# Optimization experiments

Measured on AMD Instinct MI355X. Metric: run time of the kernel, lower is better.

## Reference

```python
import jax, jax.numpy as jnp
import numpy as np

NUM_EMB = 32      # max_num_embodiments
ACTION_DIM = 32
HID = 1536        # hidden_size == input_embedding_dim
B, T = 32, 32


def sinusoidal_pos_encoding(pos, dim):
    # pos: (..., ) float positions; returns (..., dim) with interleaved sin/cos
    half = dim // 2
    div = jnp.exp(-jnp.log(10000.0) * jnp.arange(half, dtype=jnp.float32) / half)
    args = pos[..., None].astype(jnp.float32) * div  # (..., half)
    pe = jnp.stack([jnp.sin(args), jnp.cos(args)], axis=-1)  # (..., half, 2)
    return pe.reshape(*pos.shape, dim)


def cat_linear(x, W, b, cat_ids):
    # x: (B,T,Din); W: (C,Din,Dout); b: (C,Dout); cat_ids: (B,)
    # faithful to torch: gather per-sample weights then batched matmul
    Wc = W[cat_ids]                      # (B,Din,Dout)
    bc = b[cat_ids]                      # (B,Dout)
    return jnp.einsum('btd,bdh->bth', x, Wc) + bc[:, None, :]


def setup_inputs() -> dict:
    key = jax.random.key(0)
    ks = jax.random.split(key, 10)
    actions = jax.random.normal(ks[0], (B, T, ACTION_DIM), dtype=jnp.float32)
    timesteps = jax.random.randint(ks[1], (B,), 0, 1000, dtype=jnp.int32)
    cat_ids = jax.random.randint(ks[2], (B,), 0, NUM_EMB, dtype=jnp.int32)
    W1 = 0.02 * jax.random.normal(ks[3], (NUM_EMB, ACTION_DIM, HID), dtype=jnp.float32)
    b1 = jnp.zeros((NUM_EMB, HID), dtype=jnp.float32)
    W2 = 0.02 * jax.random.normal(ks[4], (NUM_EMB, 2 * HID, HID), dtype=jnp.float32)
    b2 = jnp.zeros((NUM_EMB, HID), dtype=jnp.float32)
    W3 = 0.02 * jax.random.normal(ks[5], (NUM_EMB, HID, HID), dtype=jnp.float32)
    b3 = jnp.zeros((NUM_EMB, HID), dtype=jnp.float32)
    return {"actions": actions, "timesteps": timesteps, "cat_ids": cat_ids,
            "W1": W1, "b1": b1, "W2": W2, "b2": b2, "W3": W3, "b3": b3}


def reference(actions, timesteps, cat_ids, W1, b1, W2, b2, W3, b3):
    # timesteps (B,) -> (B,T)
    ts = jnp.broadcast_to(timesteps[:, None], (actions.shape[0], actions.shape[1]))
    a_emb = cat_linear(actions, W1, b1, cat_ids)               # (B,T,HID)
    tau_emb = sinusoidal_pos_encoding(ts, HID).astype(a_emb.dtype)  # (B,T,HID)
    x = jnp.concatenate([a_emb, tau_emb], axis=-1)             # (B,T,2*HID)
    h = cat_linear(x, W2, b2, cat_ids)
    h = h * jax.nn.sigmoid(h)  # swish
    return cat_linear(h, W3, b3, cat_ids)                      # (B,T,HID)
```

## Files before the change

kernel.cpp:

```cpp
#include <hip/hip_runtime.h>
#include <hip/hip_bf16.h>
#include <cstdint>
#include <cstddef>

#define HIDD 1536
#define NB 32
#define NT 32
#define AD 32

typedef __attribute__((ext_vector_type(8))) __bf16 bf16x8;
typedef __attribute__((ext_vector_type(4))) float floatx4;

__device__ __forceinline__ unsigned short f2bf(float f) {
    union { float f; uint32_t u; } v; v.f = f;
    uint32_t r = v.u + 0x7fffu + ((v.u >> 16) & 1u);
    return (unsigned short)(r >> 16);
}

__device__ __forceinline__ uint32_t pack2(float lo, float hi) {
    return (uint32_t)f2bf(lo) | ((uint32_t)f2bf(hi) << 16);
}

__global__ __launch_bounds__(256) void build_x_kernel(
    const float* __restrict__ actions,
    const int*   __restrict__ timesteps,
    const int*   __restrict__ cat_ids,
    const float* __restrict__ W1,
    const float* __restrict__ b1,
    unsigned short* __restrict__ Xout)
{
    const int b = blockIdx.z, t = blockIdx.y;
    const int j = blockIdx.x * 256 + threadIdx.x;
    __shared__ float as[AD];
    if (threadIdx.x < AD) as[threadIdx.x] = actions[(b * NT + t) * AD + threadIdx.x];
    __syncthreads();

    float val;
    if (j < HIDD) {
        const int c = cat_ids[b];
        const float* w = W1 + ((size_t)c * AD) * HIDD + j;
        float acc = b1[c * HIDD + j];
        #pragma unroll
        for (int k = 0; k < AD; ++k) acc += as[k] * w[(size_t)k * HIDD];
        val = acc;
    } else {
        const int jj = j - HIDD;
        const int i = jj >> 1;
        const float div = expf(-9.210340371976184f * (float)i * (1.0f / 768.0f));
        const float arg = (float)timesteps[b] * div;
        val = (jj & 1) ? cosf(arg) : sinf(arg);
    }
    Xout[((size_t)(b * NT + t)) * (2 * HIDD) + j] = f2bf(val);
}

template<int K, bool SWISH>
__global__ __launch_bounds__(256) void gemm_cat_kernel(
    const unsigned short* __restrict__ X,
    const float* __restrict__ W,
    const float* __restrict__ bias,
    const int*   __restrict__ cat_ids,
    unsigned short* __restrict__ OutBf,
    float* __restrict__ OutF)
{
    const int b  = blockIdx.y;
    const int c  = cat_ids[b];
    const int n0 = blockIdx.x * 64;
    const int tid  = threadIdx.x;
    const int wave = tid >> 6;
    const int lane = tid & 63;

    __shared__ __align__(16) unsigned short Xs[32][72];
    __shared__ __align__(16) unsigned short Ws[64][72];

    floatx4 acc0 = {0.f, 0.f, 0.f, 0.f};
    floatx4 acc1 = {0.f, 0.f, 0.f, 0.f};

    const int xt = tid >> 3;
    const int xk = (tid & 7) * 8;

    const int wk_base = (tid >> 4) * 2;
    const int wn4     = (tid & 15) * 4;

    for (int kb = 0; kb < K / 64; ++kb) {
        {
            const uint4 xv = *reinterpret_cast<const uint4*>(
                X + ((size_t)(b * 32 + xt)) * K + kb * 64 + xk);
            *reinterpret_cast<uint4*>(&Xs[xt][xk]) = xv;
        }
        #pragma unroll
        for (int p = 0; p < 2; ++p) {
            const int k0 = wk_base + p * 32;
            const float* wsrc = W + ((size_t)c * K + (size_t)(kb * 64 + k0)) * HIDD + n0 + wn4;
            const float4 r0 = *reinterpret_cast<const float4*>(wsrc);
            const float4 r1 = *reinterpret_cast<const float4*>(wsrc + HIDD);
            *reinterpret_cast<uint32_t*>(&Ws[wn4 + 0][k0]) = pack2(r0.x, r1.x);
            *reinterpret_cast<uint32_t*>(&Ws[wn4 + 1][k0]) = pack2(r0.y, r1.y);
            *reinterpret_cast<uint32_t*>(&Ws[wn4 + 2][k0]) = pack2(r0.z, r1.z);
            *reinterpret_cast<uint32_t*>(&Ws[wn4 + 3][k0]) = pack2(r0.w, r1.w);
        }
        __syncthreads();

        #pragma unroll
        for (int ks = 0; ks < 2; ++ks) {
            const bf16x8 a0 = *reinterpret_cast<const bf16x8*>(
                &Xs[lane & 15][ks * 32 + (lane >> 4) * 8]);
            const bf16x8 a1 = *reinterpret_cast<const bf16x8*>(
                &Xs[16 + (lane & 15)][ks * 32 + (lane >> 4) * 8]);
            const bf16x8 bw = *reinterpret_cast<const bf16x8*>(
                &Ws[wave * 16 + (lane & 15)][ks * 32 + (lane >> 4) * 8]);
            acc0 = __builtin_amdgcn_mfma_f32_16x16x32_bf16(a0, bw, acc0, 0, 0, 0);
            acc1 = __builtin_amdgcn_mfma_f32_16x16x32_bf16(a1, bw, acc1, 0, 0, 0);
        }
        __syncthreads();
    }

    const int n_col = n0 + wave * 16 + (lane & 15);
    const float bv = bias[c * HIDD + n_col];
    const int quad = lane >> 4;
    #pragma unroll
    for (int r = 0; r < 4; ++r) {
        const int m0 = quad * 4 + r;
        float v0 = acc0[r] + bv;
        float v1 = acc1[r] + bv;
        if (SWISH) {
            v0 = v0 / (1.f + __expf(-v0));
            v1 = v1 / (1.f + __expf(-v1));
            OutBf[((size_t)(b * 32 + m0)) * HIDD + n_col] = f2bf(v0);
            OutBf[((size_t)(b * 32 + m0 + 16)) * HIDD + n_col] = f2bf(v1);
        } else {
            OutF[((size_t)(b * 32 + m0)) * HIDD + n_col] = v0;
            OutF[((size_t)(b * 32 + m0 + 16)) * HIDD + n_col] = v1;
        }
    }
}

extern "C" void kernel_launch(void* const* d_in, const int* in_sizes, int n_in,
                              void* d_out, int out_size, void* d_ws, size_t ws_size,
                              hipStream_t stream) {
    (void)in_sizes; (void)n_in; (void)out_size; (void)ws_size;
    const float* actions   = (const float*)d_in[0];
    const int*   timesteps = (const int*)d_in[1];
    const int*   cat_ids   = (const int*)d_in[2];
    const float* W1        = (const float*)d_in[3];
    const float* b1        = (const float*)d_in[4];
    const float* W2        = (const float*)d_in[5];
    const float* b2        = (const float*)d_in[6];
    const float* W3        = (const float*)d_in[7];
    const float* b3        = (const float*)d_in[8];
    float* out = (float*)d_out;

    unsigned short* xbuf = (unsigned short*)d_ws;
    unsigned short* hbuf = xbuf + (size_t)NB * NT * 2 * HIDD;

    build_x_kernel<<<dim3(12, NT, NB), 256, 0, stream>>>(
        actions, timesteps, cat_ids, W1, b1, xbuf);

    gemm_cat_kernel<2 * HIDD, true><<<dim3(24, NB), 256, 0, stream>>>(
        xbuf, W2, b2, cat_ids, hbuf, nullptr);

    gemm_cat_kernel<HIDD, false><<<dim3(24, NB), 256, 0, stream>>>(
        hbuf, W3, b3, cat_ids, nullptr, out);
}
```

Baseline: 918.4 us.

## Group samples by category so each weight tile is loaded once per group

After: 1.118 ms. 21.8% more time.

```diff
diff --git a/kernel.cpp b/kernel.cpp
--- a/kernel.cpp
+++ b/kernel.cpp
@@ -7,6 +7,8 @@
 #define NB 32
 #define NT 32
 #define AD 32
+#define NCAT 32
+#define MCHUNK 4
 
 typedef __attribute__((ext_vector_type(8))) __bf16 bf16x8;
 typedef __attribute__((ext_vector_type(4))) float floatx4;
@@ -19,6 +21,25 @@
 
 __device__ __forceinline__ uint32_t pack2(float lo, float hi) {
     return (uint32_t)f2bf(lo) | ((uint32_t)f2bf(hi) << 16);
+}
+
+__global__ void prep_kernel(const int* __restrict__ cat_ids, int* __restrict__ items) {
+    if (threadIdx.x == 0 && blockIdx.x == 0) {
+        int n = 0;
+        for (int c = 0; c < NCAT; ++c) {
+            int lst[NB]; int cnt = 0;
+            for (int b = 0; b < NB; ++b) if (cat_ids[b] == c) lst[cnt++] = b;
+            for (int off = 0; off < cnt; off += MCHUNK) {
+                int m = cnt - off; if (m > MCHUNK) m = MCHUNK;
+                items[n]      = c;
+                items[32 + n] = m;
+                for (int j = 0; j < MCHUNK; ++j)
+                    items[64 + n * 4 + j] = (j < m) ? lst[off + j] : 0;
+                ++n;
+            }
+        }
+        items[192] = n;
+    }
 }
 
 __global__ __launch_bounds__(256) void build_x_kernel(
@@ -54,82 +75,108 @@
 }
 
 template<int K, bool SWISH>
-__global__ __launch_bounds__(256) void gemm_cat_kernel(
+__global__ __launch_bounds__(256) void gemm_grouped_kernel(
     const unsigned short* __restrict__ X,
     const float* __restrict__ W,
     const float* __restrict__ bias,
-    const int*   __restrict__ cat_ids,
+    const int*   __restrict__ items,
     unsigned short* __restrict__ OutBf,
     float* __restrict__ OutF)
 {
-    const int b  = blockIdx.y;
-    const int c  = cat_ids[b];
-    const int n0 = blockIdx.x * 64;
+    const int it = blockIdx.y;
+    if (it >= items[192]) return;
+    const int c = items[it];
+    const int m = items[32 + it];
+    int smp[MCHUNK];
+    #pragma unroll
+    for (int j = 0; j < MCHUNK; ++j) smp[j] = items[64 + it * 4 + j];
+
+    const int n0   = blockIdx.x * 64;
     const int tid  = threadIdx.x;
     const int wave = tid >> 6;
     const int lane = tid & 63;
-
-    __shared__ __align__(16) unsigned short Xs[32][72];
+    const int quad = lane >> 4;
+    const int l16  = lane & 15;
+
     __shared__ __align__(16) unsigned short Ws[64][72];
 
-    floatx4 acc0 = {0.f, 0.f, 0.f, 0.f};
-    floatx4 acc1 = {0.f, 0.f, 0.f, 0.f};
-
-    const int xt = tid >> 3;
-    const int xk = (tid & 7) * 8;
-
-    const int wk_base = (tid >> 4) * 2;
-    const int wn4     = (tid & 15) * 4;
-
-    for (int kb = 0; kb < K / 64; ++kb) {
+    floatx4 acc[MCHUNK][2];
+    #pragma unroll
+    for (int si = 0; si < MCHUNK; ++si)
+        #pragma unroll
+        for (int rt = 0; rt < 2; ++rt)
+            acc[si][rt] = floatx4{0.f, 0.f, 0.f, 0.f};
+
+    const int q4 = (tid >> 4) * 4;
+    const int i4 = (tid & 15) * 4;
+    const float* wbase = W + (size_t)c * K * HIDD + n0 + i4;
+
+    constexpr int KT = K / 64;
+
+    float4 r0 = *reinterpret_cast<const float4*>(wbase + (size_t)(q4 + 0) * HIDD);
+    float4 r1 = *reinterpret_cast<const float4*>(wbase + (size_t)(q4 + 1) * HIDD);
+    float4 r2 = *reinterpret_cast<const float4*>(wbase + (size_t)(q4 + 2) * HIDD);
+    float4 r3 = *reinterpret_cast<const float4*>(wbase + (size_t)(q4 + 3) * HIDD);
+
+    for (int kb = 0; kb < KT; ++kb) {
+        __syncthreads();
         {
-            const uint4 xv = *reinterpret_cast<const uint4*>(
-                X + ((size_t)(b * 32 + xt)) * K + kb * 64 + xk);
-            *reinterpret_cast<uint4*>(&Xs[xt][xk]) = xv;
-        }
+            uint2 s0 = {pack2(r0.x, r1.x), pack2(r2.x, r3.x)};
+            uint2 s1 = {pack2(r0.y, r1.y), pack2(r2.y, r3.y)};
+            uint2 s2 = {pack2(r0.z, r1.z), pack2(r2.z, r3.z)};
+            uint2 s3 = {pack2(r0.w, r1.w), pack2(r2.w, r3.w)};
+            *reinterpret_cast<uint2*>(&Ws[i4 + 0][q4]) = s0;
+            *reinterpret_cast<uint2*>(&Ws[i4 + 1][q4]) = s1;
+            *reinterpret_cast<uint2*>(&Ws[i4 + 2][q4]) = s2;
+            *reinterpret_cast<uint2*>(&Ws[i4 + 3][q4]) = s3;
+        }
+        if (kb + 1 < KT) {
+            const float* wn = wbase + (size_t)((kb + 1) * 64 + q4) * HIDD;
+            r0 = *reinterpret_cast<const float4*>(wn);
+            r1 = *reinterpret_cast<const float4*>(wn + HIDD);
+            r2 = *reinterpret_cast<const float4*>(wn + 2 * HIDD);
+            r3 = *reinterpret_cast<const float4*>(wn + 3 * HIDD);
+        }
+        __syncthreads();
+
+        const bf16x8 bw0 = *reinterpret_cast<const bf16x8*>(&Ws[wave * 16 + l16][0 + quad * 8]);
+        const bf16x8 bw1 = *reinterpret_cast<const bf16x8*>(&Ws[wave * 16 + l16][32 + quad * 8]);
+
         #pragma unroll
-        for (int p = 0; p < 2; ++p) {
-            const int k0 = wk_base + p * 32;
-            const float* wsrc = W + ((size_t)c * K + (size_t)(kb * 64 + k0)) * HIDD + n0 + wn4;
-            const float4 r0 = *reinterpret_cast<const float4*>(wsrc);
-            const float4 r1 = *reinterpret_cast<const float4*>(wsrc + HIDD);
-            *reinterpret_cast<uint32_t*>(&Ws[wn4 + 0][k0]) = pack2(r0.x, r1.x);
-            *reinterpret_cast<uint32_t*>(&Ws[wn4 + 1][k0]) = pack2(r0.y, r1.y);
-            *reinterpret_cast<uint32_t*>(&Ws[wn4 + 2][k0]) = pack2(r0.z, r1.z);
-            *reinterpret_cast<uint32_t*>(&Ws[wn4 + 3][k0]) = pack2(r0.w, r1.w);
-        }
-        __syncthreads();
-
-        #pragma unroll
-        for (int ks = 0; ks < 2; ++ks) {
-            const bf16x8 a0 = *reinterpret_cast<const bf16x8*>(
-                &Xs[lane & 15][ks * 32 + (lane >> 4) * 8]);
-            const bf16x8 a1 = *reinterpret_cast<const bf16x8*>(
-                &Xs[16 + (lane & 15)][ks * 32 + (lane >> 4) * 8]);
-            const bf16x8 bw = *reinterpret_cast<const bf16x8*>(
-                &Ws[wave * 16 + (lane & 15)][ks * 32 + (lane >> 4) * 8]);
-            acc0 = __builtin_amdgcn_mfma_f32_16x16x32_bf16(a0, bw, acc0, 0, 0, 0);
-            acc1 = __builtin_amdgcn_mfma_f32_16x16x32_bf16(a1, bw, acc1, 0, 0, 0);
-        }
-        __syncthreads();
-    }
-
-    const int n_col = n0 + wave * 16 + (lane & 15);
+        for (int si = 0; si < MCHUNK; ++si) {
+            if (si < m) {
+                const unsigned short* xr = X + (size_t)(smp[si] * 32) * K + kb * 64 + quad * 8;
+                #pragma unroll
+                for (int rt = 0; rt < 2; ++rt) {
+                    const unsigned short* xp = xr + (size_t)(rt * 16 + l16) * K;
+                    const bf16x8 a0 = *reinterpret_cast<const bf16x8*>(xp);
+                    const bf16x8 a1 = *reinterpret_cast<const bf16x8*>(xp + 32);
+                    acc[si][rt] = __builtin_amdgcn_mfma_f32_16x16x32_bf16(a0, bw0, acc[si][rt], 0, 0, 0);
+                    acc[si][rt] = __builtin_amdgcn_mfma_f32_16x16x32_bf16(a1, bw1, acc[si][rt], 0, 0, 0);
+                }
+            }
+        }
+    }
+
+    const int n_col = n0 + wave * 16 + l16;
     const float bv = bias[c * HIDD + n_col];
-    const int quad = lane >> 4;
     #pragma unroll
-    for (int r = 0; r < 4; ++r) {
-        const int m0 = quad * 4 + r;
-        float v0 = acc0[r] + bv;
-        float v1 = acc1[r] + bv;
-        if (SWISH) {
-            v0 = v0 / (1.f + __expf(-v0));
-            v1 = v1 / (1.f + __expf(-v1));
-            OutBf[((size_t)(b * 32 + m0)) * HIDD + n_col] = f2bf(v0);
-            OutBf[((size_t)(b * 32 + m0 + 16)) * HIDD + n_col] = f2bf(v1);
-        } else {
-            OutF[((size_t)(b * 32 + m0)) * HIDD + n_col] = v0;
-            OutF[((size_t)(b * 32 + m0 + 16)) * HIDD + n_col] = v1;
+    for (int si = 0; si < MCHUNK; ++si) {
+        if (si < m) {
+            #pragma unroll
+            for (int rt = 0; rt < 2; ++rt) {
+                #pragma unroll
+                for (int r = 0; r < 4; ++r) {
+                    const int row = smp[si] * 32 + rt * 16 + quad * 4 + r;
+                    float v = acc[si][rt][r] + bv;
+                    if (SWISH) {
+                        v = v / (1.f + __expf(-v));
+                        OutBf[(size_t)row * HIDD + n_col] = f2bf(v);
+                    } else {
+                        OutF[(size_t)row * HIDD + n_col] = v;
+                    }
+                }
+            }
         }
     }
 }
@@ -149,15 +196,18 @@
     const float* b3        = (const float*)d_in[8];
     float* out = (float*)d_out;
 
-    unsigned short* xbuf = (unsigned short*)d_ws;
+    int* items = (int*)d_ws;
+    unsigned short* xbuf = (unsigned short*)d_ws + 512;
     unsigned short* hbuf = xbuf + (size_t)NB * NT * 2 * HIDD;
+
+    prep_kernel<<<1, 64, 0, stream>>>(cat_ids, items);
 
     build_x_kernel<<<dim3(12, NT, NB), 256, 0, stream>>>(
         actions, timesteps, cat_ids, W1, b1, xbuf);
 
-    gemm_cat_kernel<2 * HIDD, true><<<dim3(24, NB), 256, 0, stream>>>(
-        xbuf, W2, b2, cat_ids, hbuf, nullptr);
-
-    gemm_cat_kernel<HIDD, false><<<dim3(24, NB), 256, 0, stream>>>(
-        hbuf, W3, b3, cat_ids, nullptr, out);
-}
+    gemm_grouped_kernel<2 * HIDD, true><<<dim3(24, 32), 256, 0, stream>>>(
+        xbuf, W2, b2, items, hbuf, nullptr);
+
+    gemm_grouped_kernel<HIDD, false><<<dim3(24, 32), 256, 0, stream>>>(
+        hbuf, W3, b3, items, nullptr, out);
+}
```
